# Optimization experiments

Hardware: AMD Instinct MI355X
Metric: run time of the kernel (lower is better)

Reference implementation:

```python
import jax, jax.numpy as jnp
from jax import lax
import numpy as np


def _fps(xyz, M):
    # Farthest point sampling: sequential over M steps, vectorized over batch.
    B, N, _ = xyz.shape
    def body(carry, _):
        dists, far = carry                       # dists:[B,N], far:[B]
        c = xyz[jnp.arange(B), far]              # [B,3] current centroid
        d = jnp.sum((xyz - c[:, None, :]) ** 2, axis=-1)
        dists = jnp.minimum(dists, d)
        nxt = jnp.argmax(dists, axis=-1).astype(jnp.int32)
        return (dists, nxt), far
    init = (jnp.full((B, N), 1e10, xyz.dtype), jnp.zeros((B,), jnp.int32))
    _, inds = lax.scan(body, init, None, length=M)
    return inds.T                                # [B, M]


def _ball_query(xyz, new_xyz, radius, K):
    # For each centroid pick first K point indices within radius; pad with first hit.
    N = xyz.shape[1]
    d2 = jnp.sum((new_xyz[:, :, None, :] - xyz[:, None, :, :]) ** 2, axis=-1)  # [B,M,N]
    ids = jnp.where(d2 <= radius * radius, jnp.arange(N)[None, None, :], N)
    ids = jnp.sort(ids, axis=-1)[..., :K]        # [B,M,K]
    return jnp.where(ids == N, ids[..., :1], ids)


_gather = jax.vmap(lambda p, i: p[i])            # p:[N,C], i:[M,K] -> [M,K,C]


def _mlp(x, layers):
    # Shared per-point MLP (1x1 conv + ReLU chain); BN omitted as in source head.
    for w, b in layers:
        x = jax.nn.relu(jnp.einsum('bmkc,cd->bmkd', x, w) + b)
    return x


def _sa(xyz, points, M, radius, K, layers):
    # Set-abstraction: FPS -> ball query -> group (centered xyz ++ feats) -> MLP -> max over K.
    fi = _fps(xyz, M)                                        # [B,M]
    new_xyz = jnp.take_along_axis(xyz, fi[..., None], axis=1)  # [B,M,3]
    gi = _ball_query(xyz, new_xyz, radius, K)                # [B,M,K]
    g_xyz = _gather(xyz, gi) - new_xyz[:, :, None, :]        # [B,M,K,3]
    g = jnp.concatenate([g_xyz, _gather(points, gi)], axis=-1)
    return new_xyz, jnp.max(_mlp(g, layers), axis=2)         # [B,M,Cout]


def _forward(xyz, points,
             w1a, b1a, w1b, b1b, w1c, b1c,
             w2a, b2a, w2b, b2b, w2c, b2c,
             w3a, b3a, w3b, b3b, w3c, b3c,
             lin1_w, lin2_w, cls_w, cls_b):
    B = xyz.shape[0]
    x1, f1 = _sa(xyz, points, 512, 0.2, 32, [(w1a, b1a), (w1b, b1b), (w1c, b1c)])
    x2, f2 = _sa(x1, f1, 128, 0.4, 64, [(w2a, b2a), (w2b, b2b), (w2c, b2c)])
    # group_all: single group containing all 128 points, feats = [xyz ++ points] (259 ch)
    g = jnp.concatenate([x2, f2], axis=-1)[:, None]           # [B,1,128,259]
    f3 = jnp.max(_mlp(g, [(w3a, b3a), (w3b, b3b), (w3c, b3c)]), axis=2)  # [B,1,1024]
    net = f3.reshape(B, -1)
    net = jax.nn.relu(net @ lin1_w)   # linear1 (no bias) + ReLU; dropout=identity (eval)
    net = jax.nn.relu(net @ lin2_w)
    return net @ cls_w + cls_b


def setup_inputs() -> dict:
    key = jax.random.key(0)
    ks = iter(jax.random.split(key, 40))
    B, N, NC = 32, 1024, 40
    inp = {}
    inp['xyz'] = jax.random.uniform(next(ks), (B, N, 3), jnp.float32, -1.0, 1.0)
    inp['points'] = jax.random.normal(next(ks), (B, N, 3), jnp.float32)
    def lin(cin, cout):
        w = jax.random.normal(next(ks), (cin, cout), jnp.float32) / np.float32(np.sqrt(cin))
        return w, jnp.zeros((cout,), jnp.float32)
    dims = {'1': [(6, 64), (64, 64), (64, 128)],
            '2': [(131, 128), (128, 128), (128, 256)],
            '3': [(259, 256), (256, 512), (512, 1024)]}
    for s, layer_dims in dims.items():
        for tag, (ci, co) in zip('abc', layer_dims):
            w, b = lin(ci, co)
            inp['w%s%s' % (s, tag)] = w
            inp['b%s%s' % (s, tag)] = b
    inp['lin1_w'] = jax.random.normal(next(ks), (1024, 512), jnp.float32) / np.float32(32.0)
    inp['lin2_w'] = jax.random.normal(next(ks), (512, 256), jnp.float32) / np.float32(np.sqrt(512))
    inp['cls_w'] = jax.random.normal(next(ks), (256, NC), jnp.float32) / np.float32(16.0)
    inp['cls_b'] = jnp.zeros((NC,), jnp.float32)
    return inp


def reference(xyz, points,
              w1a, b1a, w1b, b1b, w1c, b1c,
              w2a, b2a, w2b, b2b, w2c, b2c,
              w3a, b3a, w3b, b3b, w3c, b3c,
              lin1_w, lin2_w, cls_w, cls_b):
    return _forward(xyz, points,
                    w1a, b1a, w1b, b1b, w1c, b1c,
                    w2a, b2a, w2b, b2b, w2c, b2c,
                    w3a, b3a, w3b, b3b, w3c, b3c,
                    lin1_w, lin2_w, cls_w, cls_b)
```

## Files before the change

### kernel.cpp

```cpp
#include <hip/hip_runtime.h>

#define DEVFN __device__ __forceinline__

static inline int ceil_div(int a, int b) { return (a + b - 1) / b; }

typedef __attribute__((ext_vector_type(8))) short         bf16x8;
typedef __attribute__((ext_vector_type(4))) float         f32x4;
typedef __attribute__((ext_vector_type(8))) unsigned short u16x8;

DEVFN unsigned short f2bf(float x) {
    unsigned u = __float_as_uint(x);
    unsigned r = ((u >> 16) & 1u) + 0x7fffu;
    return (unsigned short)((u + r) >> 16);
}
DEVFN float bf2f(unsigned short h) { return __uint_as_float(((unsigned)h) << 16); }

template<int CTRL>
DEVFN double dpp_max_step(double v)
{
    int lo = __double2loint(v), hi = __double2hiint(v);
    int tlo = __builtin_amdgcn_update_dpp(lo, lo, CTRL, 0xF, 0xF, false);
    int thi = __builtin_amdgcn_update_dpp(hi, hi, CTRL, 0xF, 0xF, false);
    return fmax(v, __hiloint2double(thi, tlo));
}

template<int N>
__global__ __launch_bounds__(64) void fps_kernel(const float* __restrict__ xyz, int M,
                                                 int* __restrict__ out_idx,
                                                 float* __restrict__ nxout)
{
    constexpr int PPL = N / 64;
    int b = blockIdx.x, lane = threadIdx.x;
    __shared__ float4 sp[N];
    const float* p = xyz + (size_t)b * N * 3;
    float px[PPL], py[PPL], pz[PPL], dd[PPL];
    unsigned lo[PPL];
    #pragma unroll
    for (int j = 0; j < PPL; ++j) {
        int idx = lane + 64 * j;
        px[j] = p[idx*3+0]; py[j] = p[idx*3+1]; pz[j] = p[idx*3+2];
        sp[idx] = make_float4(px[j], py[j], pz[j], 0.f);
        dd[j] = 1e10f;
        lo[j] = ~(unsigned)idx;
    }
    __syncthreads();
    int far = 0;
    for (int s = 0; s < M; ++s) {
        float4 c4 = sp[far];
        if (lane == 0) {
            out_idx[(size_t)b*M + s] = far;
            nxout[((size_t)b*M + s)*3 + 0] = c4.x;
            nxout[((size_t)b*M + s)*3 + 1] = c4.y;
            nxout[((size_t)b*M + s)*3 + 2] = c4.z;
        }
        double cand[PPL];
        #pragma unroll
        for (int j = 0; j < PPL; ++j) {
            float dx = __fsub_rn(px[j], c4.x);
            float dy = __fsub_rn(py[j], c4.y);
            float dz = __fsub_rn(pz[j], c4.z);
            float d  = __fadd_rn(__fadd_rn(__fmul_rn(dx,dx), __fmul_rn(dy,dy)),
                                 __fmul_rn(dz,dz));
            float nd = fminf(dd[j], d);
            dd[j] = nd;
            cand[j] = __hiloint2double(__float_as_int(nd), (int)lo[j]);
        }
        #pragma unroll
        for (int st = PPL/2; st > 0; st >>= 1)
            #pragma unroll
            for (int j = 0; j < PPL; ++j)
                if (j < st) cand[j] = fmax(cand[j], cand[j + st]);
        double v = cand[0];
        v = dpp_max_step<0xB1>(v);
        v = dpp_max_step<0x4E>(v);
        v = dpp_max_step<0x124>(v);
        v = dpp_max_step<0x128>(v);
        v = dpp_max_step<0x142>(v);
        v = dpp_max_step<0x143>(v);
        int wlo = __builtin_amdgcn_readlane(__double2loint(v), 63);
        far = (int)(~(unsigned)wlo);
    }
}

__global__ void ballquery_kernel(const float* __restrict__ xyz,
                                 const float* __restrict__ new_xyz,
                                 int* __restrict__ gi,
                                 int B, int N, int M, int K, float r2)
{
    int t = blockIdx.x * blockDim.x + threadIdx.x;
    if (t >= B * M) return;
    int b = t / M;
    const float* p = xyz + (size_t)b * N * 3;
    float cx = new_xyz[t*3+0], cy = new_xyz[t*3+1], cz = new_xyz[t*3+2];
    int* out = gi + (size_t)t * K;
    int cnt = 0, first = 0;
    bool havefirst = false;
    for (int i = 0; i < N; ++i) {
        float dx = __fsub_rn(p[i*3+0], cx);
        float dy = __fsub_rn(p[i*3+1], cy);
        float dz = __fsub_rn(p[i*3+2], cz);
        float d  = __fadd_rn(__fadd_rn(__fmul_rn(dx,dx), __fmul_rn(dy,dy)),
                             __fmul_rn(dz,dz));
        if (d <= r2) {
            if (!havefirst) { first = i; havefirst = true; }
            out[cnt++] = i;
            if (cnt == K) break;
        }
    }
    for (; cnt < K; ++cnt) out[cnt] = first;
}

DEVFN float f4_elem(const float4& v, int u) {
    return u == 0 ? v.x : u == 1 ? v.y : u == 2 ? v.z : v.w;
}

__global__ void wsplit_kernel(const float* __restrict__ w,
                              unsigned short* __restrict__ wh,
                              unsigned short* __restrict__ wl,
                              int CItot, int CO, int CIpad, int ro)
{
    int t = blockIdx.x * 256 + threadIdx.x;
    if (t >= CIpad * CO) return;
    int co = t / CIpad, ci = t % CIpad;
    int src = ci + ro;
    float v = (src < CItot) ? w[(size_t)src * CO + co] : 0.f;
    unsigned short h = f2bf(v);
    wh[t] = h;
    wl[t] = f2bf(v - bf2f(h));
}

template<int CF, int CO, int KPTS>
__global__ __launch_bounds__(256) void sa_l1_kernel(
    const float* __restrict__ xyz, const float* __restrict__ feats,
    const float* __restrict__ new_xyz, const int* __restrict__ gi,
    const float* __restrict__ w, const float* __restrict__ bias,
    unsigned short* __restrict__ oh, unsigned short* __restrict__ ol,
    int N, int M, int row0)
{
    constexpr int WCH = CO / 4;
    const int lane = threadIdx.x & 63;
    const int wv   = __builtin_amdgcn_readfirstlane(threadIdx.x >> 6);
    const int rl   = blockIdx.x * 64 + lane;
    const int row  = row0 + rl;
    const int cent = row / KPTS;
    const int b    = cent / M;
    const int idx  = gi[row];
    const float* pp  = xyz + ((size_t)b*N + idx)*3;
    const float* cc3 = new_xyz + (size_t)cent*3;
    float a0 = __fsub_rn(pp[0], cc3[0]);
    float a1 = __fsub_rn(pp[1], cc3[1]);
    float a2 = __fsub_rn(pp[2], cc3[2]);
    const float* frow = feats + ((size_t)b*N + idx)*CF;
    const float* wcol = w + wv*WCH;
    const float* bcol = bias + wv*WCH;
    float acc[WCH];
    #pragma unroll
    for (int j = 0; j < WCH; ++j) acc[j] = bcol[j];
    #pragma unroll
    for (int j = 0; j < WCH; ++j) acc[j] += a0 * wcol[0*CO + j];
    #pragma unroll
    for (int j = 0; j < WCH; ++j) acc[j] += a1 * wcol[1*CO + j];
    #pragma unroll
    for (int j = 0; j < WCH; ++j) acc[j] += a2 * wcol[2*CO + j];
    constexpr int CF4 = CF & ~3;
    #pragma unroll 2
    for (int cc = 0; cc < CF4; cc += 4) {
        float4 a4 = *(const float4*)(frow + cc);
        #pragma unroll
        for (int u = 0; u < 4; ++u) {
            float a = f4_elem(a4, u);
            #pragma unroll
            for (int j = 0; j < WCH; ++j)
                acc[j] += a * wcol[(size_t)(3 + cc + u)*CO + j];
        }
    }
    #pragma unroll
    for (int f = CF4; f < CF; ++f) {
        float a = frow[f];
        #pragma unroll
        for (int j = 0; j < WCH; ++j)
            acc[j] += a * wcol[(size_t)(3 + f)*CO + j];
    }
    #pragma unroll
    for (int j8 = 0; j8 < WCH; j8 += 8) {
        u16x8 hv, lv;
        #pragma unroll
        for (int u = 0; u < 8; ++u) {
            float v = fmaxf(acc[j8+u], 0.f);
            unsigned short h = f2bf(v);
            hv[u] = (unsigned short)h;
            lv[u] = f2bf(v - bf2f(h));
        }
        size_t o = (size_t)rl*CO + wv*WCH + j8;
        *(u16x8*)(&oh[o]) = hv;
        *(u16x8*)(&ol[o]) = lv;
    }
}

template<int CI, int CO, int NTILE, int MROW, int KPTS, int OUTMODE>
__global__ __launch_bounds__(256) void mfma_layer_kernel(
    const unsigned short* __restrict__ ah, const unsigned short* __restrict__ al,
    const unsigned short* __restrict__ wh, const unsigned short* __restrict__ wl,
    const float* __restrict__ bias,
    unsigned short* __restrict__ oh, unsigned short* __restrict__ ol,
    float* __restrict__ ofp, int rowbase)
{
    constexpr int KT = CI / 32;
    static_assert(KT * MROW <= 18, "A-preload register budget");
    __shared__ float partial[4][OUTMODE >= 2 ? MROW : 1][OUTMODE >= 2 ? 16*NTILE : 1];
    const int wid  = threadIdx.x >> 6;
    const int lane = threadIdx.x & 63;
    const int m    = lane & 15;
    const int kg   = lane >> 4;
    const int blockrow = blockIdx.x * (64 * MROW);
    const int colbase  = blockIdx.y * (16 * NTILE);
    bf16x8 Ahf[MROW * KT], Alf[MROW * KT];
    #pragma unroll
    for (int t = 0; t < MROW; ++t) {
        const unsigned short* arh =
            ah + (size_t)(blockrow + t*64 + wid*16 + m) * CI + kg * 8;
        const unsigned short* arl =
            al + (size_t)(blockrow + t*64 + wid*16 + m) * CI + kg * 8;
        #pragma unroll
        for (int kt = 0; kt < KT; ++kt) {
            Ahf[t*KT + kt] = *(const bf16x8*)(arh + kt*32);
            Alf[t*KT + kt] = *(const bf16x8*)(arl + kt*32);
        }
    }
    #pragma unroll
    for (int nt = 0; nt < NTILE; ++nt) {
        f32x4 acc[MROW];
        #pragma unroll
        for (int t = 0; t < MROW; ++t) acc[t] = (f32x4){0.f, 0.f, 0.f, 0.f};
        const unsigned short* wbh = wh + (size_t)(colbase + nt*16 + m) * CI + kg * 8;
        const unsigned short* wbl = wl + (size_t)(colbase + nt*16 + m) * CI + kg * 8;
        #pragma unroll
        for (int kt = 0; kt < KT; ++kt) {
            bf16x8 Bh = *(const bf16x8*)(wbh + kt*32);
            bf16x8 Bl = *(const bf16x8*)(wbl + kt*32);
            #pragma unroll
            for (int t = 0; t < MROW; ++t) {
                acc[t] = __builtin_amdgcn_mfma_f32_16x16x32_bf16(Ahf[t*KT+kt], Bh, acc[t], 0, 0, 0);
                acc[t] = __builtin_amdgcn_mfma_f32_16x16x32_bf16(Ahf[t*KT+kt], Bl, acc[t], 0, 0, 0);
                acc[t] = __builtin_amdgcn_mfma_f32_16x16x32_bf16(Alf[t*KT+kt], Bh, acc[t], 0, 0, 0);
            }
        }
        int dcol = colbase + nt*16 + m;
        float bv = bias[dcol];
        #pragma unroll
        for (int t = 0; t < MROW; ++t) {
            float v[4];
            #pragma unroll
            for (int r = 0; r < 4; ++r) v[r] = fmaxf(acc[t][r] + bv, 0.f);
            if constexpr (OUTMODE == 0) {
                #pragma unroll
                for (int r = 0; r < 4; ++r) {
                    size_t o = (size_t)(blockrow + t*64 + wid*16 + kg*4 + r) * CO + dcol;
                    unsigned short h = f2bf(v[r]);
                    oh[o] = h;
                    ol[o] = f2bf(v[r] - bf2f(h));
                }
            } else if constexpr (OUTMODE == 1) {
                #pragma unroll
                for (int r = 0; r < 4; ++r)
                    ofp[(size_t)(blockrow + t*64 + wid*16 + kg*4 + r) * CO + dcol] = v[r];
            } else {
                float mx = fmaxf(fmaxf(v[0], v[1]), fmaxf(v[2], v[3]));
                mx = fmaxf(mx, __shfl_xor(mx, 16));
                mx = fmaxf(mx, __shfl_xor(mx, 32));
                if (lane < 16) partial[wid][t][nt*16 + m] = mx;
            }
        }
    }
    if constexpr (OUTMODE >= 2) {
        __syncthreads();
        for (int c = threadIdx.x; c < 16*NTILE; c += 256) {
            #pragma unroll
            for (int t = 0; t < MROW; ++t) {
                if constexpr (KPTS == 64) {
                    float mx = fmaxf(fmaxf(partial[0][t][c], partial[1][t][c]),
                                     fmaxf(partial[2][t][c], partial[3][t][c]));
                    int cent = (rowbase + blockrow) / 64 + t;
                    if constexpr (OUTMODE == 2) {
                        ofp[(size_t)cent*CO + colbase + c] = mx;
                    } else {
                        size_t o = (size_t)cent*CO + colbase + c;
                        unsigned short h = f2bf(mx);
                        oh[o] = h; ol[o] = f2bf(mx - bf2f(h));
                    }
                } else {
                    int cent0 = (rowbase + blockrow) / 32 + t*2;
                    float v0 = fmaxf(partial[0][t][c], partial[1][t][c]);
                    float v1 = fmaxf(partial[2][t][c], partial[3][t][c]);
                    if constexpr (OUTMODE == 2) {
                        ofp[(size_t)cent0*CO + colbase + c]     = v0;
                        ofp[(size_t)(cent0+1)*CO + colbase + c] = v1;
                    } else {
                        size_t o0 = (size_t)cent0*CO + colbase + c;
                        size_t o1 = (size_t)(cent0+1)*CO + colbase + c;
                        unsigned short h0 = f2bf(v0), h1 = f2bf(v1);
                        oh[o0] = h0; ol[o0] = f2bf(v0 - bf2f(h0));
                        oh[o1] = h1; ol[o1] = f2bf(v1 - bf2f(h1));
                    }
                }
            }
        }
    }
}

template<int NTILE, int MROW>
__global__ __launch_bounds__(256) void mfma_sa2l1_kernel(
    const float* __restrict__ sxyz,
    const float* __restrict__ cxyz,
    const int* __restrict__ gi,
    const unsigned short* __restrict__ f1h, const unsigned short* __restrict__ f1l,
    const float* __restrict__ w,
    const unsigned short* __restrict__ wh, const unsigned short* __restrict__ wl,
    const float* __restrict__ bias,
    unsigned short* __restrict__ oh, unsigned short* __restrict__ ol,
    int rowbase)
{
    constexpr int CI = 128, CO = 128, KT = 4, KPTS = 64, M = 128, N = 512;
    const int wid  = threadIdx.x >> 6;
    const int lane = threadIdx.x & 63;
    const int m    = lane & 15;
    const int kg   = lane >> 4;
    const int blockrow = blockIdx.x * (64 * MROW);
    const int colbase  = blockIdx.y * (16 * NTILE);
    bf16x8 Ahf[MROW * KT], Alf[MROW * KT];
    #pragma unroll
    for (int t = 0; t < MROW; ++t) {
        int grow = rowbase + blockrow + t*64 + wid*16 + m;
        int cent = grow / KPTS;
        int b    = cent / M;
        int idx  = gi[grow];
        const unsigned short* arh = f1h + ((size_t)b*N + idx) * CI + kg * 8;
        const unsigned short* arl = f1l + ((size_t)b*N + idx) * CI + kg * 8;
        #pragma unroll
        for (int kt = 0; kt < KT; ++kt) {
            Ahf[t*KT + kt] = *(const bf16x8*)(arh + kt*32);
            Alf[t*KT + kt] = *(const bf16x8*)(arl + kt*32);
        }
    }
    float dx[MROW][4], dy[MROW][4], dz[MROW][4];
    #pragma unroll
    for (int t = 0; t < MROW; ++t)
        #pragma unroll
        for (int r = 0; r < 4; ++r) {
            int grow = rowbase + blockrow + t*64 + wid*16 + kg*4 + r;
            int cent = grow / KPTS;
            int b    = cent / M;
            int idx  = gi[grow];
            const float* pp = sxyz + ((size_t)b*N + idx)*3;
            const float* cc = cxyz + (size_t)cent*3;
            dx[t][r] = __fsub_rn(pp[0], cc[0]);
            dy[t][r] = __fsub_rn(pp[1], cc[1]);
            dz[t][r] = __fsub_rn(pp[2], cc[2]);
        }
    #pragma unroll
    for (int nt = 0; nt < NTILE; ++nt) {
        f32x4 acc[MROW];
        #pragma unroll
        for (int t = 0; t < MROW; ++t) acc[t] = (f32x4){0.f, 0.f, 0.f, 0.f};
        const unsigned short* wbh = wh + (size_t)(colbase + nt*16 + m) * CI + kg * 8;
        const unsigned short* wbl = wl + (size_t)(colbase + nt*16 + m) * CI + kg * 8;
        #pragma unroll
        for (int kt = 0; kt < KT; ++kt) {
            bf16x8 Bh = *(const bf16x8*)(wbh + kt*32);
            bf16x8 Bl = *(const bf16x8*)(wbl + kt*32);
            #pragma unroll
            for (int t = 0; t < MROW; ++t) {
                acc[t] = __builtin_amdgcn_mfma_f32_16x16x32_bf16(Ahf[t*KT+kt], Bh, acc[t], 0, 0, 0);
                acc[t] = __builtin_amdgcn_mfma_f32_16x16x32_bf16(Ahf[t*KT+kt], Bl, acc[t], 0, 0, 0);
                acc[t] = __builtin_amdgcn_mfma_f32_16x16x32_bf16(Alf[t*KT+kt], Bh, acc[t], 0, 0, 0);
            }
        }
        int dcol = colbase + nt*16 + m;
        float w0 = w[0*CO + dcol], w1 = w[1*CO + dcol], w2 = w[2*CO + dcol];
        float bv = bias[dcol];
        #pragma unroll
        for (int t = 0; t < MROW; ++t)
            #pragma unroll
            for (int r = 0; r < 4; ++r) {
                float v = acc[t][r] + bv + dx[t][r]*w0 + dy[t][r]*w1 + dz[t][r]*w2;
                v = fmaxf(v, 0.f);
                size_t o = (size_t)(blockrow + t*64 + wid*16 + kg*4 + r) * CO + dcol;
                unsigned short h = f2bf(v);
                oh[o] = h;
                ol[o] = f2bf(v - bf2f(h));
            }
    }
}

__global__ void concat_split_kernel(const float* __restrict__ a, const float* __restrict__ f,
                                    unsigned short* __restrict__ oh,
                                    unsigned short* __restrict__ ol,
                                    int R, int CF, int CIpad)
{
    int t = blockIdx.x * 256 + threadIdx.x;
    if (t >= R * CIpad) return;
    int r = t / CIpad, c = t % CIpad;
    float v;
    if (c < 3) v = a[r*3 + c];
    else if (c < CF + 3) v = f[(size_t)r * CF + (c - 3)];
    else v = 0.f;
    unsigned short h = f2bf(v);
    oh[t] = h;
    ol[t] = f2bf(v - bf2f(h));
}

template<int RELU, int HASB>
__global__ __launch_bounds__(256) void fc_kernel(
    const float* __restrict__ A, const float* __restrict__ W,
    const float* __restrict__ bias, float* __restrict__ Cc,
    int Mr, int Nc, int Kd)
{
    int t = blockIdx.x * 256 + threadIdx.x;
    if (t >= Mr * Nc) return;
    int row = t / Nc, col = t % Nc;
    const float* a = A + (size_t)row * Kd;
    const float* w = W + col;
    float acc = 0.f;
    #pragma unroll 8
    for (int k = 0; k < Kd; ++k)
        acc += a[k] * w[(size_t)k * Nc];
    if (HASB) acc += bias[col];
    if (RELU) acc = fmaxf(acc, 0.f);
    Cc[t] = acc;
}

__global__ void rowmax_kernel(const float* __restrict__ in, float* __restrict__ out,
                              int B, int P, int C)
{
    int t = blockIdx.x * blockDim.x + threadIdx.x;
    if (t >= B * C) return;
    int b = t / C, c = t % C;
    const float* p = in + (size_t)b * P * C + c;
    float mx = p[0];
    for (int i = 1; i < P; ++i) mx = fmaxf(mx, p[(size_t)i * C]);
    out[t] = mx;
}

extern "C" void kernel_launch(void* const* d_in, const int* in_sizes, int n_in,
                              void* d_out, int out_size, void* d_ws, size_t ws_size,
                              hipStream_t stream)
{
    const float* xyz    = (const float*)d_in[0];
    const float* points = (const float*)d_in[1];
    const float* w1a = (const float*)d_in[2];  const float* b1a = (const float*)d_in[3];
    const float* w1b = (const float*)d_in[4];  const float* b1b = (const float*)d_in[5];
    const float* w1c = (const float*)d_in[6];  const float* b1c = (const float*)d_in[7];
    const float* w2a = (const float*)d_in[8];  const float* b2a = (const float*)d_in[9];
    const float* w2b = (const float*)d_in[10]; const float* b2b = (const float*)d_in[11];
    const float* w2c = (const float*)d_in[12]; const float* b2c = (const float*)d_in[13];
    const float* w3a = (const float*)d_in[14]; const float* b3a = (const float*)d_in[15];
    const float* w3b = (const float*)d_in[16]; const float* b3b = (const float*)d_in[17];
    const float* w3c = (const float*)d_in[18]; const float* b3c = (const float*)d_in[19];
    const float* lin1 = (const float*)d_in[20];
    const float* lin2 = (const float*)d_in[21];
    const float* clsw = (const float*)d_in[22];
    const float* clsb = (const float*)d_in[23];

    char* ws = (char*)d_ws;
    size_t off = 0;
    auto alloc = [&](size_t bytes) -> void* {
        void* p = ws + off;
        off += (bytes + 255) & ~(size_t)255;
        return p;
    };
    int*   fps1 = (int*)  alloc((size_t)32*512*4);
    float* nx1  = (float*)alloc((size_t)32*512*3*4);
    int*   gi1  = (int*)  alloc((size_t)32*512*32*4);
    int*   fps2 = (int*)  alloc((size_t)32*128*4);
    float* nx2  = (float*)alloc((size_t)32*128*3*4);
    int*   gi2  = (int*)  alloc((size_t)32*128*64*4);
    float* f2   = (float*)alloc((size_t)32*128*256*4);
    float* h3c  = (float*)alloc((size_t)4096*1024*4);
    float* f3   = (float*)alloc((size_t)32*1024*4);
    float* fc1  = (float*)alloc((size_t)32*512*4);
    float* fc2  = (float*)alloc((size_t)32*256*4);

    typedef unsigned short us;
    us* w1bh = (us*)alloc(64*64*2);     us* w1bl = (us*)alloc(64*64*2);
    us* w1ch = (us*)alloc(128*64*2);    us* w1cl = (us*)alloc(128*64*2);
    us* w2ah = (us*)alloc(128*128*2);   us* w2al = (us*)alloc(128*128*2);
    us* w2bh = (us*)alloc(128*128*2);   us* w2bl = (us*)alloc(128*128*2);
    us* w2ch = (us*)alloc(256*128*2);   us* w2cl = (us*)alloc(256*128*2);
    us* w3ah = (us*)alloc(256*288*2);   us* w3al = (us*)alloc(256*288*2);
    us* w3bh = (us*)alloc(512*256*2);   us* w3bl = (us*)alloc(512*256*2);
    us* w3ch = (us*)alloc(1024*512*2);  us* w3cl = (us*)alloc(1024*512*2);
    us* f1h  = (us*)alloc((size_t)16384*128*2);
    us* f1l  = (us*)alloc((size_t)16384*128*2);
    us* g3H  = (us*)alloc((size_t)4096*288*2);  us* g3L  = (us*)alloc((size_t)4096*288*2);
    us* h3aH = (us*)alloc((size_t)4096*256*2);  us* h3aL = (us*)alloc((size_t)4096*256*2);
    us* h3bH = (us*)alloc((size_t)4096*512*2);  us* h3bL = (us*)alloc((size_t)4096*512*2);

    size_t avail = (ws_size > off + 1024) ? (ws_size - off - 1024) : 0;
    size_t bufcap = avail / 4;
    if (bufcap > (size_t)67200000) bufcap = 67200000;
    us* Ah = (us*)alloc(bufcap); us* Al = (us*)alloc(bufcap);
    us* Bh = (us*)alloc(bufcap); us* Bl = (us*)alloc(bufcap);

    auto wsp = [&](const float* w, int CItot, int CO, int CIpad, int ro, us* wh, us* wl) {
        wsplit_kernel<<<ceil_div(CIpad*CO, 256), 256, 0, stream>>>(w, wh, wl, CItot, CO, CIpad, ro);
    };
    wsp(w1b, 64, 64, 64, 0,   w1bh, w1bl);
    wsp(w1c, 64, 128, 64, 0,  w1ch, w1cl);
    wsp(w2a, 131, 128, 128, 3, w2ah, w2al);
    wsp(w2b, 128, 128, 128, 0, w2bh, w2bl);
    wsp(w2c, 128, 256, 128, 0, w2ch, w2cl);
    wsp(w3a, 259, 256, 288, 0, w3ah, w3al);
    wsp(w3b, 256, 512, 256, 0, w3bh, w3bl);
    wsp(w3c, 512, 1024, 512, 0, w3ch, w3cl);

    fps_kernel<1024><<<32, 64, 0, stream>>>(xyz, 512, fps1, nx1);
    ballquery_kernel<<<ceil_div(32*512, 256), 256, 0, stream>>>(
        xyz, nx1, gi1, 32, 1024, 512, 32, (float)(0.2*0.2));
    {
        const int rows = 32*512*32;
        int ch = (int)((bufcap / (64*2)) & ~(size_t)1023);
        if (ch > rows) ch = rows;
        if (ch < 1024) ch = 1024;
        for (int r0 = 0; r0 < rows; r0 += ch) {
            int rc = rows - r0 < ch ? rows - r0 : ch;
            sa_l1_kernel<3, 64, 32><<<rc/64, 256, 0, stream>>>(
                xyz, points, nx1, gi1, w1a, b1a, Ah, Al, 1024, 512, r0);
            mfma_layer_kernel<64, 64, 4, 4, 0, 0><<<dim3(rc/256, 1), 256, 0, stream>>>(
                Ah, Al, w1bh, w1bl, b1b, Bh, Bl, nullptr, 0);
            mfma_layer_kernel<64, 128, 8, 4, 32, 3><<<dim3(rc/256, 1), 256, 0, stream>>>(
                Bh, Bl, w1ch, w1cl, b1c, f1h, f1l, nullptr, r0);
        }
    }

    fps_kernel<512><<<32, 64, 0, stream>>>(nx1, 128, fps2, nx2);
    ballquery_kernel<<<ceil_div(32*128, 256), 256, 0, stream>>>(
        nx1, nx2, gi2, 32, 512, 128, 64, (float)(0.4*0.4));
    {
        const int rows = 32*128*64;
        int ch = (int)((bufcap / (128*2)) & ~(size_t)1023);
        if (ch > rows) ch = rows;
        if (ch < 1024) ch = 1024;
        for (int r0 = 0; r0 < rows; r0 += ch) {
            int rc = rows - r0 < ch ? rows - r0 : ch;
            mfma_sa2l1_kernel<8, 2><<<dim3(rc/128, 1), 256, 0, stream>>>(
                nx1, nx2, gi2, f1h, f1l, w2a, w2ah, w2al, b2a, Ah, Al, r0);
            mfma_layer_kernel<128, 128, 8, 4, 0, 0><<<dim3(rc/256, 1), 256, 0, stream>>>(
                Ah, Al, w2bh, w2bl, b2b, Bh, Bl, nullptr, 0);
            mfma_layer_kernel<128, 256, 16, 4, 64, 2><<<dim3(rc/256, 1), 256, 0, stream>>>(
                Bh, Bl, w2ch, w2cl, b2c, nullptr, nullptr, f2, r0);
        }
    }

    concat_split_kernel<<<ceil_div(4096*288, 256), 256, 0, stream>>>(
        nx2, f2, g3H, g3L, 4096, 256, 288);
    mfma_layer_kernel<288, 256, 2, 1, 0, 0><<<dim3(4096/64, 256/32), 256, 0, stream>>>(
        g3H, g3L, w3ah, w3al, b3a, h3aH, h3aL, nullptr, 0);
    mfma_layer_kernel<256, 512, 2, 2, 0, 0><<<dim3(4096/128, 512/32), 256, 0, stream>>>(
        h3aH, h3aL, w3bh, w3bl, b3b, h3bH, h3bL, nullptr, 0);
    mfma_layer_kernel<512, 1024, 4, 1, 0, 1><<<dim3(4096/64, 1024/64), 256, 0, stream>>>(
        h3bH, h3bL, w3ch, w3cl, b3c, nullptr, nullptr, h3c, 0);
    rowmax_kernel<<<ceil_div(32*1024, 256), 256, 0, stream>>>(h3c, f3, 32, 128, 1024);

    fc_kernel<1,0><<<ceil_div(32*512, 256), 256, 0, stream>>>(
        f3, lin1, nullptr, fc1, 32, 512, 1024);
    fc_kernel<1,0><<<ceil_div(32*256, 256), 256, 0, stream>>>(
        fc1, lin2, nullptr, fc2, 32, 256, 512);
    fc_kernel<0,1><<<ceil_div(32*40, 256), 256, 0, stream>>>(
        fc2, clsw, clsb, (float*)d_out, 32, 40, 256);
}
```

Baseline: 1.262 ms.

## Overlap SA2 farthest-point sampling and ball query with SA1 MLP kernels

The second-stage FPS (32 blocks) now runs as extra blocks of the first SA1 layer kernel, and the second-stage ball query runs as extra blocks of the SA1 layer-2 MFMA kernel. This hides the serial, low-occupancy FPS and ball-query work behind the large SA1 MLP launches and removes two separate launches. The SA1 first layer is also specialised with constants and a fused per-column loop. The risk is that the long FPS blocks become the critical path of the first kernel and delay the next launch, and the fused work only happens on the first chunk iteration.

```diff
diff --git a/kernel.cpp b/kernel.cpp
--- a/kernel.cpp
+++ b/kernel.cpp
@@ -7,13 +7,14 @@
 typedef __attribute__((ext_vector_type(8))) short         bf16x8;
 typedef __attribute__((ext_vector_type(4))) float         f32x4;
 typedef __attribute__((ext_vector_type(8))) unsigned short u16x8;
-
-DEVFN unsigned short f2bf(float x) {
+typedef unsigned short us;
+
+DEVFN us f2bf(float x) {
     unsigned u = __float_as_uint(x);
     unsigned r = ((u >> 16) & 1u) + 0x7fffu;
-    return (unsigned short)((u + r) >> 16);
-}
-DEVFN float bf2f(unsigned short h) { return __uint_as_float(((unsigned)h) << 16); }
+    return (us)((u + r) >> 16);
+}
+DEVFN float bf2f(us h) { return __uint_as_float(((unsigned)h) << 16); }
 
 template<int CTRL>
 DEVFN double dpp_max_step(double v)
@@ -115,8 +116,7 @@
 }
 
 __global__ void wsplit_kernel(const float* __restrict__ w,
-                              unsigned short* __restrict__ wh,
-                              unsigned short* __restrict__ wl,
+                              us* __restrict__ wh, us* __restrict__ wl,
                               int CItot, int CO, int CIpad, int ro)
 {
     int t = blockIdx.x * 256 + threadIdx.x;
@@ -124,20 +124,79 @@
     int co = t / CIpad, ci = t % CIpad;
     int src = ci + ro;
     float v = (src < CItot) ? w[(size_t)src * CO + co] : 0.f;
-    unsigned short h = f2bf(v);
+    us h = f2bf(v);
     wh[t] = h;
     wl[t] = f2bf(v - bf2f(h));
 }
 
-template<int CF, int CO, int KPTS>
-__global__ __launch_bounds__(256) void sa_l1_kernel(
+__global__ __launch_bounds__(256) void sa1_l1_fps2_kernel(
     const float* __restrict__ xyz, const float* __restrict__ feats,
-    const float* __restrict__ new_xyz, const int* __restrict__ gi,
+    const float* __restrict__ new_xyz , const int* __restrict__ gi,
     const float* __restrict__ w, const float* __restrict__ bias,
-    unsigned short* __restrict__ oh, unsigned short* __restrict__ ol,
-    int N, int M, int row0)
-{
-    constexpr int WCH = CO / 4;
+    us* __restrict__ oh, us* __restrict__ ol,
+    int row0, int nb_main, int fps_on,
+    int* __restrict__ fps2, float* __restrict__ nx2)
+{
+    __shared__ float4 sp[512];
+    if ((int)blockIdx.x >= nb_main) {
+        if (!fps_on) return;
+        constexpr int N = 512, PPL = 8, MS = 128;
+        const int b   = blockIdx.x - nb_main;
+        const int tid = threadIdx.x, lane = tid & 63;
+        float px[PPL], py[PPL], pz[PPL], dd[PPL];
+        unsigned lo[PPL];
+        if (tid < 64) {
+            const float* p = new_xyz + (size_t)b * N * 3;
+            #pragma unroll
+            for (int j = 0; j < PPL; ++j) {
+                int idx = lane + 64 * j;
+                px[j] = p[idx*3+0]; py[j] = p[idx*3+1]; pz[j] = p[idx*3+2];
+                sp[idx] = make_float4(px[j], py[j], pz[j], 0.f);
+                dd[j] = 1e10f;
+                lo[j] = ~(unsigned)idx;
+            }
+        }
+        __syncthreads();
+        if (tid >= 64) return;
+        int far = 0;
+        for (int s = 0; s < MS; ++s) {
+            float4 c4 = sp[far];
+            if (lane == 0) {
+                fps2[(size_t)b*MS + s] = far;
+                nx2[((size_t)b*MS + s)*3 + 0] = c4.x;
+                nx2[((size_t)b*MS + s)*3 + 1] = c4.y;
+                nx2[((size_t)b*MS + s)*3 + 2] = c4.z;
+            }
+            double cand[PPL];
+            #pragma unroll
+            for (int j = 0; j < PPL; ++j) {
+                float dx = __fsub_rn(px[j], c4.x);
+                float dy = __fsub_rn(py[j], c4.y);
+                float dz = __fsub_rn(pz[j], c4.z);
+                float d  = __fadd_rn(__fadd_rn(__fmul_rn(dx,dx), __fmul_rn(dy,dy)),
+                                     __fmul_rn(dz,dz));
+                float nd = fminf(dd[j], d);
+                dd[j] = nd;
+                cand[j] = __hiloint2double(__float_as_int(nd), (int)lo[j]);
+            }
+            #pragma unroll
+            for (int st = PPL/2; st > 0; st >>= 1)
+                #pragma unroll
+                for (int j = 0; j < PPL; ++j)
+                    if (j < st) cand[j] = fmax(cand[j], cand[j + st]);
+            double v = cand[0];
+            v = dpp_max_step<0xB1>(v);
+            v = dpp_max_step<0x4E>(v);
+            v = dpp_max_step<0x124>(v);
+            v = dpp_max_step<0x128>(v);
+            v = dpp_max_step<0x142>(v);
+            v = dpp_max_step<0x143>(v);
+            int wlo = __builtin_amdgcn_readlane(__double2loint(v), 63);
+            far = (int)(~(unsigned)wlo);
+        }
+        return;
+    }
+    constexpr int CF = 3, CO = 64, KPTS = 32, N = 1024, M = 512, WCH = 16;
     const int lane = threadIdx.x & 63;
     const int wv   = __builtin_amdgcn_readfirstlane(threadIdx.x >> 6);
     const int rl   = blockIdx.x * 64 + lane;
@@ -151,35 +210,20 @@
     float a1 = __fsub_rn(pp[1], cc3[1]);
     float a2 = __fsub_rn(pp[2], cc3[2]);
     const float* frow = feats + ((size_t)b*N + idx)*CF;
+    float f0 = frow[0], f1v = frow[1], f2v = frow[2];
     const float* wcol = w + wv*WCH;
     const float* bcol = bias + wv*WCH;
     float acc[WCH];
     #pragma unroll
-    for (int j = 0; j < WCH; ++j) acc[j] = bcol[j];
-    #pragma unroll
-    for (int j = 0; j < WCH; ++j) acc[j] += a0 * wcol[0*CO + j];
-    #pragma unroll
-    for (int j = 0; j < WCH; ++j) acc[j] += a1 * wcol[1*CO + j];
-    #pragma unroll
-    for (int j = 0; j < WCH; ++j) acc[j] += a2 * wcol[2*CO + j];
-    constexpr int CF4 = CF & ~3;
-    #pragma unroll 2
-    for (int cc = 0; cc < CF4; cc += 4) {
-        float4 a4 = *(const float4*)(frow + cc);
-        #pragma unroll
-        for (int u = 0; u < 4; ++u) {
-            float a = f4_elem(a4, u);
-            #pragma unroll
-            for (int j = 0; j < WCH; ++j)
-                acc[j] += a * wcol[(size_t)(3 + cc + u)*CO + j];
-        }
-    }
-    #pragma unroll
-    for (int f = CF4; f < CF; ++f) {
-        float a = frow[f];
-        #pragma unroll
-        for (int j = 0; j < WCH; ++j)
-            acc[j] += a * wcol[(size_t)(3 + f)*CO + j];
+    for (int j = 0; j < WCH; ++j) {
+        float a = bcol[j];
+        a += a0 * wcol[0*CO + j];
+        a += a1 * wcol[1*CO + j];
+        a += a2 * wcol[2*CO + j];
+        a += f0 * wcol[3*CO + j];
+        a += f1v * wcol[4*CO + j];
+        a += f2v * wcol[5*CO + j];
+        acc[j] = a;
     }
     #pragma unroll
     for (int j8 = 0; j8 < WCH; j8 += 8) {
@@ -187,8 +231,8 @@
         #pragma unroll
         for (int u = 0; u < 8; ++u) {
             float v = fmaxf(acc[j8+u], 0.f);
-            unsigned short h = f2bf(v);
-            hv[u] = (unsigned short)h;
+            us h = f2bf(v);
+            hv[u] = h;
             lv[u] = f2bf(v - bf2f(h));
         }
         size_t o = (size_t)rl*CO + wv*WCH + j8;
@@ -197,12 +241,98 @@
     }
 }
 
+__global__ __launch_bounds__(256) void sa1_l2_bq2_kernel(
+    const us* __restrict__ ah, const us* __restrict__ al,
+    const us* __restrict__ wh, const us* __restrict__ wl,
+    const float* __restrict__ bias,
+    us* __restrict__ oh, us* __restrict__ ol,
+    int nb_main, int bq_on,
+    const float* __restrict__ nx1, const float* __restrict__ nx2,
+    int* __restrict__ gi2)
+{
+    if ((int)blockIdx.x >= nb_main) {
+        if (!bq_on) return;
+        int t = (blockIdx.x - nb_main) * 256 + threadIdx.x;
+        if (t >= 32 * 128) return;
+        constexpr int N = 512, M = 128, K = 64;
+        const float r2 = (float)(0.4*0.4);
+        int b = t / M;
+        const float* p = nx1 + (size_t)b * N * 3;
+        float cx = nx2[t*3+0], cy = nx2[t*3+1], cz = nx2[t*3+2];
+        int* out = gi2 + (size_t)t * K;
+        int cnt = 0, first = 0;
+        bool havefirst = false;
+        for (int i = 0; i < N; ++i) {
+            float dx = __fsub_rn(p[i*3+0], cx);
+            float dy = __fsub_rn(p[i*3+1], cy);
+            float dz = __fsub_rn(p[i*3+2], cz);
+            float d  = __fadd_rn(__fadd_rn(__fmul_rn(dx,dx), __fmul_rn(dy,dy)),
+                                 __fmul_rn(dz,dz));
+            if (d <= r2) {
+                if (!havefirst) { first = i; havefirst = true; }
+                out[cnt++] = i;
+                if (cnt == K) break;
+            }
+        }
+        for (; cnt < K; ++cnt) out[cnt] = first;
+        return;
+    }
+    constexpr int CI = 64, CO = 64, KT = 2, NTILE = 4, MROW = 4;
+    const int wid  = threadIdx.x >> 6;
+    const int lane = threadIdx.x & 63;
+    const int m    = lane & 15;
+    const int kg   = lane >> 4;
+    const int blockrow = blockIdx.x * (64 * MROW);
+    bf16x8 Ahf[MROW * KT], Alf[MROW * KT];
+    #pragma unroll
+    for (int t = 0; t < MROW; ++t) {
+        const us* arh = ah + (size_t)(blockrow + t*64 + wid*16 + m) * CI + kg * 8;
+        const us* arl = al + (size_t)(blockrow + t*64 + wid*16 + m) * CI + kg * 8;
+        #pragma unroll
+        for (int kt = 0; kt < KT; ++kt) {
+            Ahf[t*KT + kt] = *(const bf16x8*)(arh + kt*32);
+            Alf[t*KT + kt] = *(const bf16x8*)(arl + kt*32);
+        }
+    }
+    #pragma unroll
+    for (int nt = 0; nt < NTILE; ++nt) {
+        f32x4 acc[MROW];
+        #pragma unroll
+        for (int t = 0; t < MROW; ++t) acc[t] = (f32x4){0.f, 0.f, 0.f, 0.f};
+        const us* wbh = wh + (size_t)(nt*16 + m) * CI + kg * 8;
+        const us* wbl = wl + (size_t)(nt*16 + m) * CI + kg * 8;
+        #pragma unroll
+        for (int kt = 0; kt < KT; ++kt) {
+            bf16x8 Bh = *(const bf16x8*)(wbh + kt*32);
+            bf16x8 Bl = *(const bf16x8*)(wbl + kt*32);
+            #pragma unroll
+            for (int t = 0; t < MROW; ++t) {
+                acc[t] = __builtin_amdgcn_mfma_f32_16x16x32_bf16(Ahf[t*KT+kt], Bh, acc[t], 0, 0, 0);
+                acc[t] = __builtin_amdgcn_mfma_f32_16x16x32_bf16(Ahf[t*KT+kt], Bl, acc[t], 0, 0, 0);
+                acc[t] = __builtin_amdgcn_mfma_f32_16x16x32_bf16(Alf[t*KT+kt], Bh, acc[t], 0, 0, 0);
+            }
+        }
+        int dcol = nt*16 + m;
+        float bv = bias[dcol];
+        #pragma unroll
+        for (int t = 0; t < MROW; ++t)
+            #pragma unroll
+            for (int r = 0; r < 4; ++r) {
+                float v = fmaxf(acc[t][r] + bv, 0.f);
+                size_t o = (size_t)(blockrow + t*64 + wid*16 + kg*4 + r) * CO + dcol;
+                us h = f2bf(v);
+                oh[o] = h;
+                ol[o] = f2bf(v - bf2f(h));
+            }
+    }
+}
+
 template<int CI, int CO, int NTILE, int MROW, int KPTS, int OUTMODE>
 __global__ __launch_bounds__(256) void mfma_layer_kernel(
-    const unsigned short* __restrict__ ah, const unsigned short* __restrict__ al,
-    const unsigned short* __restrict__ wh, const unsigned short* __restrict__ wl,
+    const us* __restrict__ ah, const us* __restrict__ al,
+    const us* __restrict__ wh, const us* __restrict__ wl,
     const float* __restrict__ bias,
-    unsigned short* __restrict__ oh, unsigned short* __restrict__ ol,
+    us* __restrict__ oh, us* __restrict__ ol,
     float* __restrict__ ofp, int rowbase)
 {
     constexpr int KT = CI / 32;
@@ -217,10 +347,8 @@
     bf16x8 Ahf[MROW * KT], Alf[MROW * KT];
     #pragma unroll
     for (int t = 0; t < MROW; ++t) {
-        const unsigned short* arh =
-            ah + (size_t)(blockrow + t*64 + wid*16 + m) * CI + kg * 8;
-        const unsigned short* arl =
-            al + (size_t)(blockrow + t*64 + wid*16 + m) * CI + kg * 8;
+        const us* arh = ah + (size_t)(blockrow + t*64 + wid*16 + m) * CI + kg * 8;
+        const us* arl = al + (size_t)(blockrow + t*64 + wid*16 + m) * CI + kg * 8;
         #pragma unroll
         for (int kt = 0; kt < KT; ++kt) {
             Ahf[t*KT + kt] = *(const bf16x8*)(arh + kt*32);
@@ -232,8 +360,8 @@
         f32x4 acc[MROW];
         #pragma unroll
         for (int t = 0; t < MROW; ++t) acc[t] = (f32x4){0.f, 0.f, 0.f, 0.f};
-        const unsigned short* wbh = wh + (size_t)(colbase + nt*16 + m) * CI + kg * 8;
-        const unsigned short* wbl = wl + (size_t)(colbase + nt*16 + m) * CI + kg * 8;
+        const us* wbh = wh + (size_t)(colbase + nt*16 + m) * CI + kg * 8;
+        const us* wbl = wl + (size_t)(colbase + nt*16 + m) * CI + kg * 8;
         #pragma unroll
         for (int kt = 0; kt < KT; ++kt) {
             bf16x8 Bh = *(const bf16x8*)(wbh + kt*32);
@@ -256,7 +384,7 @@
                 #pragma unroll
                 for (int r = 0; r < 4; ++r) {
                     size_t o = (size_t)(blockrow + t*64 + wid*16 + kg*4 + r) * CO + dcol;
-                    unsigned short h = f2bf(v[r]);
+                    us h = f2bf(v[r]);
                     oh[o] = h;
                     ol[o] = f2bf(v[r] - bf2f(h));
                 }
@@ -285,7 +413,7 @@
                         ofp[(size_t)cent*CO + colbase + c] = mx;
                     } else {
                         size_t o = (size_t)cent*CO + colbase + c;
-                        unsigned short h = f2bf(mx);
+                        us h = f2bf(mx);
                         oh[o] = h; ol[o] = f2bf(mx - bf2f(h));
                     }
                 } else {
@@ -298,7 +426,7 @@
                     } else {
                         size_t o0 = (size_t)cent0*CO + colbase + c;
                         size_t o1 = (size_t)(cent0+1)*CO + colbase + c;
-                        unsigned short h0 = f2bf(v0), h1 = f2bf(v1);
+                        us h0 = f2bf(v0), h1 = f2bf(v1);
                         oh[o0] = h0; ol[o0] = f2bf(v0 - bf2f(h0));
                         oh[o1] = h1; ol[o1] = f2bf(v1 - bf2f(h1));
                     }
@@ -310,14 +438,13 @@
 
 template<int NTILE, int MROW>
 __global__ __launch_bounds__(256) void mfma_sa2l1_kernel(
-    const float* __restrict__ sxyz,
-    const float* __restrict__ cxyz,
+    const float* __restrict__ sxyz, const float* __restrict__ cxyz,
     const int* __restrict__ gi,
-    const unsigned short* __restrict__ f1h, const unsigned short* __restrict__ f1l,
+    const us* __restrict__ f1h, const us* __restrict__ f1l,
     const float* __restrict__ w,
-    const unsigned short* __restrict__ wh, const unsigned short* __restrict__ wl,
+    const us* __restrict__ wh, const us* __restrict__ wl,
     const float* __restrict__ bias,
-    unsigned short* __restrict__ oh, unsigned short* __restrict__ ol,
+    us* __restrict__ oh, us* __restrict__ ol,
     int rowbase)
 {
     constexpr int CI = 128, CO = 128, KT = 4, KPTS = 64, M = 128, N = 512;
@@ -334,8 +461,8 @@
         int cent = grow / KPTS;
         int b    = cent / M;
         int idx  = gi[grow];
-        const unsigned short* arh = f1h + ((size_t)b*N + idx) * CI + kg * 8;
-        const unsigned short* arl = f1l + ((size_t)b*N + idx) * CI + kg * 8;
+        const us* arh = f1h + ((size_t)b*N + idx) * CI + kg * 8;
+        const us* arl = f1l + ((size_t)b*N + idx) * CI + kg * 8;
         #pragma unroll
         for (int kt = 0; kt < KT; ++kt) {
             Ahf[t*KT + kt] = *(const bf16x8*)(arh + kt*32);
@@ -362,8 +489,8 @@
         f32x4 acc[MROW];
         #pragma unroll
         for (int t = 0; t < MROW; ++t) acc[t] = (f32x4){0.f, 0.f, 0.f, 0.f};
-        const unsigned short* wbh = wh + (size_t)(colbase + nt*16 + m) * CI + kg * 8;
-        const unsigned short* wbl = wl + (size_t)(colbase + nt*16 + m) * CI + kg * 8;
+        const us* wbh = wh + (size_t)(colbase + nt*16 + m) * CI + kg * 8;
+        const us* wbl = wl + (size_t)(colbase + nt*16 + m) * CI + kg * 8;
         #pragma unroll
         for (int kt = 0; kt < KT; ++kt) {
             bf16x8 Bh = *(const bf16x8*)(wbh + kt*32);
@@ -385,7 +512,7 @@
                 float v = acc[t][r] + bv + dx[t][r]*w0 + dy[t][r]*w1 + dz[t][r]*w2;
                 v = fmaxf(v, 0.f);
                 size_t o = (size_t)(blockrow + t*64 + wid*16 + kg*4 + r) * CO + dcol;
-                unsigned short h = f2bf(v);
+                us h = f2bf(v);
                 oh[o] = h;
                 ol[o] = f2bf(v - bf2f(h));
             }
@@ -393,8 +520,7 @@
 }
 
 __global__ void concat_split_kernel(const float* __restrict__ a, const float* __restrict__ f,
-                                    unsigned short* __restrict__ oh,
-                                    unsigned short* __restrict__ ol,
+                                    us* __restrict__ oh, us* __restrict__ ol,
                                     int R, int CF, int CIpad)
 {
     int t = blockIdx.x * 256 + threadIdx.x;
@@ -404,7 +530,7 @@
     if (c < 3) v = a[r*3 + c];
     else if (c < CF + 3) v = f[(size_t)r * CF + (c - 3)];
     else v = 0.f;
-    unsigned short h = f2bf(v);
+    us h = f2bf(v);
     oh[t] = h;
     ol[t] = f2bf(v - bf2f(h));
 }
@@ -480,7 +606,6 @@
     float* fc1  = (float*)alloc((size_t)32*512*4);
     float* fc2  = (float*)alloc((size_t)32*256*4);
 
-    typedef unsigned short us;
     us* w1bh = (us*)alloc(64*64*2);     us* w1bl = (us*)alloc(64*64*2);
     us* w1ch = (us*)alloc(128*64*2);    us* w1cl = (us*)alloc(128*64*2);
     us* w2ah = (us*)alloc(128*128*2);   us* w2al = (us*)alloc(128*128*2);
@@ -521,20 +646,20 @@
         int ch = (int)((bufcap / (64*2)) & ~(size_t)1023);
         if (ch > rows) ch = rows;
         if (ch < 1024) ch = 1024;
+        int first = 1;
         for (int r0 = 0; r0 < rows; r0 += ch) {
             int rc = rows - r0 < ch ? rows - r0 : ch;
-            sa_l1_kernel<3, 64, 32><<<rc/64, 256, 0, stream>>>(
-                xyz, points, nx1, gi1, w1a, b1a, Ah, Al, 1024, 512, r0);
-            mfma_layer_kernel<64, 64, 4, 4, 0, 0><<<dim3(rc/256, 1), 256, 0, stream>>>(
-                Ah, Al, w1bh, w1bl, b1b, Bh, Bl, nullptr, 0);
-            mfma_layer_kernel<64, 128, 8, 4, 32, 3><<<dim3(rc/256, 1), 256, 0, stream>>>(
+            int nb1 = rc/64, nb2 = rc/256;
+            sa1_l1_fps2_kernel<<<nb1 + (first ? 32 : 0), 256, 0, stream>>>(
+                xyz, points, nx1, gi1, w1a, b1a, Ah, Al, r0, nb1, first, fps2, nx2);
+            sa1_l2_bq2_kernel<<<nb2 + (first ? 16 : 0), 256, 0, stream>>>(
+                Ah, Al, w1bh, w1bl, b1b, Bh, Bl, nb2, first, nx1, nx2, gi2);
+            mfma_layer_kernel<64, 128, 8, 4, 32, 3><<<dim3(nb2, 1), 256, 0, stream>>>(
                 Bh, Bl, w1ch, w1cl, b1c, f1h, f1l, nullptr, r0);
-        }
-    }
-
-    fps_kernel<512><<<32, 64, 0, stream>>>(nx1, 128, fps2, nx2);
-    ballquery_kernel<<<ceil_div(32*128, 256), 256, 0, stream>>>(
-        nx1, nx2, gi2, 32, 512, 128, 64, (float)(0.4*0.4));
+            first = 0;
+        }
+    }
+
     {
         const int rows = 32*128*64;
         int ch = (int)((bufcap / (128*2)) & ~(size_t)1023);
```

Result: no change. 1.253 ms (-0.7%).
